# Kernel optimization log

Measured on AMD Instinct MI355X. Metric: run time of the kernel, lower is better.

The kernel has to match this reference:

```python
import jax, jax.numpy as jnp
import numpy as np

V, E = 4096, 8192
HV, HE, OUT = 256, 128, 256
EPS = 1e-6


def _one_hot_incidence(idx, n_rows, n_cols):
    # incidence matrix M[v, e] = 1 if idx[e] == v
    return jnp.zeros((n_rows, n_cols), jnp.float32).at[idx, jnp.arange(n_cols)].set(1.0)


def setup_inputs() -> dict:
    key = jax.random.key(0)
    ks = jax.random.split(key, 12)
    # edge endpoints: first V source indices cover every vertex -> positive degrees
    u_idx = jnp.concatenate([jnp.arange(V), jax.random.randint(ks[0], (E - V,), 0, V)])
    v_idx = jax.random.randint(ks[1], (E,), 0, V)
    vew1 = _one_hot_incidence(u_idx, V, E)
    vew2 = _one_hot_incidence(v_idx, V, E)
    hv_ftr = jax.random.normal(ks[2], (V, HV), jnp.float32)
    he_ftr = jax.random.normal(ks[3], (E, HE), jnp.float32)
    s = lambda d: 1.0 / np.sqrt(d)
    w_att = jax.random.normal(ks[4], (HV + HE + HV, 1), jnp.float32) * s(HV + HE + HV)
    b_att = jnp.zeros((1,), jnp.float32)
    w_gcn = jax.random.normal(ks[5], (HV, HV), jnp.float32) * s(HV)
    b_gcn = jnp.zeros((HV,), jnp.float32)
    w1 = jax.random.normal(ks[6], (2 * HV, HV), jnp.float32) * s(2 * HV)
    b1 = jnp.zeros((HV,), jnp.float32)
    w2 = jax.random.normal(ks[7], (HV, OUT), jnp.float32) * s(HV)
    b2 = jnp.zeros((OUT,), jnp.float32)
    return dict(hv_ftr=hv_ftr, he_ftr=he_ftr, vew1=vew1, vew2=vew2,
                w_att=w_att, b_att=b_att, w_gcn=w_gcn, b_gcn=b_gcn,
                w1=w1, b1=b1, w2=w2, b2=b2)


def reference(hv_ftr, he_ftr, vew1, vew2, w_att, b_att, w_gcn, b_gcn, w1, b1, w2, b2):
    vew_u = jnp.concatenate([vew1, vew2], axis=1)  # [V, 2E]
    vew_v = jnp.concatenate([vew2, vew1], axis=1)  # [V, 2E]
    hv_u = vew_u.T @ hv_ftr                         # [2E, HV] gather of source feats
    hv_v = vew_v.T @ hv_ftr                         # [2E, HV] gather of target feats
    he2 = jnp.concatenate([he_ftr, he_ftr], axis=0)  # [2E, HE]
    uev = jnp.concatenate([hv_u, he2, hv_v], axis=1)  # [2E, 2HV+HE]
    edge_w = jax.nn.sigmoid(uev @ w_att + b_att).reshape(-1)  # [2E]
    adj = vew_u @ (vew_v * edge_w[None, :]).T       # [V, V]
    # normalize_adj_rc: D_r^{-1/2} A D_c^{-1/2}
    d_r = jax.lax.rsqrt(jnp.maximum(adj.sum(axis=1), EPS))
    d_c = jax.lax.rsqrt(jnp.maximum(adj.sum(axis=0), EPS))
    adj_n = adj * d_r[:, None] * d_c[None, :]
    # GCN(hv_dim->hv_dim, tanh): propagate linear-transformed features
    hidden = jnp.tanh(adj_n @ (hv_ftr @ w_gcn + b_gcn))  # [V, HV]
    # MLP remap: [hv, hidden] -> hidden_dim HV -> OUT (dropout off at inference)
    h = jnp.concatenate([hv_ftr, hidden], axis=1)   # [V, 2HV]
    h = jax.nn.leaky_relu(h @ w1 + b1)
    return h @ w2 + b2                               # [V, OUT]
```

## Files before the change

kernel.cpp:

```cpp
#include <hip/hip_runtime.h>
#include <hip/hip_bf16.h>
#include <math.h>

#define V 4096
#define E 8192
#define HV 256
#define HE 128
#define OUT_DIM 256
#define EPS 1e-6f

typedef __attribute__((ext_vector_type(8))) short short8;
typedef __attribute__((ext_vector_type(4))) float f32x4;

__device__ __forceinline__ unsigned short f2bf(float f) {
    __hip_bfloat16 h = __float2bfloat16(f);
    return *(unsigned short*)&h;
}

__global__ __launch_bounds__(256) void zero_kernel(float4* __restrict__ p, int n4) {
    int i = blockIdx.x * blockDim.x + threadIdx.x;
    int stride = gridDim.x * blockDim.x;
    float4 z = {0.0f, 0.0f, 0.0f, 0.0f};
    for (; i < n4; i += stride) p[i] = z;
}

__global__ __launch_bounds__(256) void idx_kernel(const float4* __restrict__ m,
                                                  int* __restrict__ out) {
    const int EQ = E / 4;
    const size_t total = (size_t)V * EQ;
    for (size_t i = (size_t)blockIdx.x * blockDim.x + threadIdx.x; i < total;
         i += (size_t)gridDim.x * blockDim.x) {
        float4 x = m[i];
        if (x.x + x.y + x.z + x.w > 0.5f) {
            int v  = (int)(i / EQ);
            int c4 = (int)(i % EQ) * 4;
            if (x.x > 0.5f) out[c4 + 0] = v;
            if (x.y > 0.5f) out[c4 + 1] = v;
            if (x.z > 0.5f) out[c4 + 2] = v;
            if (x.w > 0.5f) out[c4 + 3] = v;
        }
    }
}

__global__ __launch_bounds__(256) void conv_kernel(const float4* __restrict__ src,
                                                   ushort4* __restrict__ dst, int n4) {
    int i = blockIdx.x * blockDim.x + threadIdx.x;
    int stride = gridDim.x * blockDim.x;
    for (; i < n4; i += stride) {
        float4 x = src[i];
        ushort4 o;
        o.x = f2bf(x.x); o.y = f2bf(x.y); o.z = f2bf(x.z); o.w = f2bf(x.w);
        dst[i] = o;
    }
}

__global__ __launch_bounds__(256) void convT_kernel(const float* __restrict__ src,
                                                    unsigned short* __restrict__ dst,
                                                    int K, int N) {
    int i = blockIdx.x * blockDim.x + threadIdx.x;
    if (i >= N * K) return;
    int n = i / K, k = i - n * K;
    dst[i] = f2bf(src[(size_t)k * N + n]);
}

__global__ __launch_bounds__(64) void proj_kernel(const float* __restrict__ hv,
                                                  const float* __restrict__ he,
                                                  const float* __restrict__ watt,
                                                  float* __restrict__ pu,
                                                  float* __restrict__ pv,
                                                  float* __restrict__ pe) {
    int r = blockIdx.x;
    int lane = threadIdx.x;
    if (r < V) {
        float4 x  = *(const float4*)(hv + (size_t)r * HV + lane * 4);
        float4 wu = *(const float4*)(watt + lane * 4);
        float4 wv = *(const float4*)(watt + HV + HE + lane * 4);
        float su = x.x * wu.x + x.y * wu.y + x.z * wu.z + x.w * wu.w;
        float sv = x.x * wv.x + x.y * wv.y + x.z * wv.z + x.w * wv.w;
        #pragma unroll
        for (int o = 32; o > 0; o >>= 1) {
            su += __shfl_down(su, o);
            sv += __shfl_down(sv, o);
        }
        if (lane == 0) { pu[r] = su; pv[r] = sv; }
    } else {
        int e = r - V;
        float2 x = *(const float2*)(he + (size_t)e * HE + lane * 2);
        float2 w = *(const float2*)(watt + HV + lane * 2);
        float s = x.x * w.x + x.y * w.y;
        #pragma unroll
        for (int o = 32; o > 0; o >>= 1) s += __shfl_down(s, o);
        if (lane == 0) pe[e] = s;
    }
}

__global__ __launch_bounds__(256) void edge_kernel(const int* __restrict__ iu,
                                                   const int* __restrict__ iv,
                                                   const float* __restrict__ pu,
                                                   const float* __restrict__ pv,
                                                   const float* __restrict__ pe,
                                                   const float* __restrict__ batt,
                                                   float* __restrict__ ew,
                                                   float* __restrict__ dr,
                                                   float* __restrict__ dc) {
    int e2 = blockIdx.x * blockDim.x + threadIdx.x;
    if (e2 >= 2 * E) return;
    int e  = (e2 < E) ? e2 : e2 - E;
    int uu = (e2 < E) ? iu[e] : iv[e];
    int vv = (e2 < E) ? iv[e] : iu[e];
    float x = pu[uu] + pe[e] + pv[vv] + batt[0];
    float w = 1.0f / (1.0f + expf(-x));
    ew[e2] = w;
    atomicAdd(dr + uu, w);
    atomicAdd(dc + vv, w);
}

template <int ACT, int OBF>
__global__ __launch_bounds__(256) void gemm_bf16(const unsigned short* __restrict__ A0,
                                                 const unsigned short* __restrict__ A1,
                                                 int KSEG, int NSEG,
                                                 const unsigned short* __restrict__ BT,
                                                 const float* __restrict__ bias,
                                                 void* __restrict__ Cout,
                                                 int M, int N) {
    __shared__ __align__(16) unsigned short As[64 * 40];
    __shared__ __align__(16) unsigned short Bs[64 * 40];
    const int tid  = threadIdx.x;
    const int lane = tid & 63;
    const int w    = tid >> 6;
    const int wm   = w >> 1, wn = w & 1;
    const int bm   = blockIdx.y * 64, bn = blockIdx.x * 64;
    const int Ktot = KSEG * NSEG;

    const int sr = tid >> 2;
    const int sc = (tid & 3) * 8;
    const int fr = lane & 15;
    const int kc = (lane >> 4) * 8;

    f32x4 acc[2][2] = {};

    for (int k0 = 0; k0 < Ktot; k0 += 32) {
        int seg = (k0 >= KSEG) ? 1 : 0;
        int kk  = k0 - seg * KSEG;
        const unsigned short* Asrc = seg ? A1 : A0;
        *(short8*)&As[sr * 40 + sc] = *(const short8*)&Asrc[(size_t)(bm + sr) * KSEG + kk + sc];
        *(short8*)&Bs[sr * 40 + sc] = *(const short8*)&BT[(size_t)(bn + sr) * Ktot + k0 + sc];
        __syncthreads();
        short8 bfr[2];
        bfr[0] = *(const short8*)&Bs[(wn * 32 + 0 * 16 + fr) * 40 + kc];
        bfr[1] = *(const short8*)&Bs[(wn * 32 + 1 * 16 + fr) * 40 + kc];
        #pragma unroll
        for (int ms = 0; ms < 2; ++ms) {
            short8 af = *(const short8*)&As[(wm * 32 + ms * 16 + fr) * 40 + kc];
            acc[ms][0] = __builtin_amdgcn_mfma_f32_16x16x32_bf16(af, bfr[0], acc[ms][0], 0, 0, 0);
            acc[ms][1] = __builtin_amdgcn_mfma_f32_16x16x32_bf16(af, bfr[1], acc[ms][1], 0, 0, 0);
        }
        __syncthreads();
    }

    #pragma unroll
    for (int ms = 0; ms < 2; ++ms) {
        #pragma unroll
        for (int ns = 0; ns < 2; ++ns) {
            int col = bn + wn * 32 + ns * 16 + fr;
            float bv = bias ? bias[col] : 0.0f;
            #pragma unroll
            for (int r = 0; r < 4; ++r) {
                int row = bm + wm * 32 + ms * 16 + ((lane >> 4) << 2) + r;
                float v = acc[ms][ns][r] + bv;
                if (ACT == 1) v = (v > 0.0f) ? v : 0.01f * v;
                if (OBF) ((unsigned short*)Cout)[(size_t)row * N + col] = f2bf(v);
                else     ((float*)Cout)[(size_t)row * N + col] = v;
            }
        }
    }
}

__global__ __launch_bounds__(64) void scatter_kernel(const int* __restrict__ iu,
                                                     const int* __restrict__ iv,
                                                     const float* __restrict__ ew,
                                                     const float* __restrict__ dc,
                                                     const float* __restrict__ X,
                                                     float* __restrict__ acc) {
    int e2 = blockIdx.x;
    int t  = threadIdx.x;
    int e  = (e2 < E) ? e2 : e2 - E;
    int uu = (e2 < E) ? iu[e] : iv[e];
    int vv = (e2 < E) ? iv[e] : iu[e];
    float coef = ew[e2] * rsqrtf(fmaxf(dc[vv], EPS));
    float4 x = *(const float4*)(X + (size_t)vv * HV + t * 4);
    float* dst = acc + (size_t)uu * HV + t * 4;
    atomicAdd(dst + 0, coef * x.x);
    atomicAdd(dst + 1, coef * x.y);
    atomicAdd(dst + 2, coef * x.z);
    atomicAdd(dst + 3, coef * x.w);
}

__global__ __launch_bounds__(256) void finish_kernel(const float* __restrict__ dr,
                                                     const float* __restrict__ acc,
                                                     unsigned short* __restrict__ hid16) {
    const size_t total = (size_t)V * HV;
    for (size_t idx = (size_t)blockIdx.x * blockDim.x + threadIdx.x; idx < total;
         idx += (size_t)gridDim.x * blockDim.x) {
        int row = (int)(idx >> 8);
        float s = rsqrtf(fmaxf(dr[row], EPS));
        hid16[idx] = f2bf(tanhf(s * acc[idx]));
    }
}

extern "C" void kernel_launch(void* const* d_in, const int* in_sizes, int n_in,
                              void* d_out, int out_size, void* d_ws, size_t ws_size,
                              hipStream_t stream) {
    const float* hv   = (const float*)d_in[0];
    const float* he   = (const float*)d_in[1];
    const float* vew1 = (const float*)d_in[2];
    const float* vew2 = (const float*)d_in[3];
    const float* watt = (const float*)d_in[4];
    const float* batt = (const float*)d_in[5];
    const float* wgcn = (const float*)d_in[6];
    const float* bgcn = (const float*)d_in[7];
    const float* w1   = (const float*)d_in[8];
    const float* b1   = (const float*)d_in[9];
    const float* w2   = (const float*)d_in[10];
    const float* b2   = (const float*)d_in[11];
    float* out = (float*)d_out;

    float* ws = (float*)d_ws;
    int*   iu  = (int*)ws;
    int*   iv  = (int*)(ws + E);
    float* pu  = ws + 2 * E;
    float* pv  = pu + V;
    float* pe  = pv + V;
    float* ew  = pe + E;
    float* dr  = ew + 2 * E;
    float* dc  = dr + V;
    float* acc = dc + V;
    float* X   = acc + (size_t)V * HV;
    unsigned short* hv16  = (unsigned short*)(X + (size_t)V * HV);
    unsigned short* hid16 = hv16 + (size_t)V * HV;
    unsigned short* t16   = hid16 + (size_t)V * HV;
    unsigned short* wgcnT = t16 + (size_t)V * HV;
    unsigned short* w1T   = wgcnT + HV * HV;
    unsigned short* w2T   = w1T + 2 * HV * HV;

    zero_kernel<<<1024, 256, 0, stream>>>((float4*)dr, (2 * V + V * HV) / 4);

    idx_kernel<<<2048, 256, 0, stream>>>((const float4*)vew1, iu);
    idx_kernel<<<2048, 256, 0, stream>>>((const float4*)vew2, iv);

    conv_kernel<<<512, 256, 0, stream>>>((const float4*)hv, (ushort4*)hv16, V * HV / 4);
    convT_kernel<<<(HV * HV + 255) / 256, 256, 0, stream>>>(wgcn, wgcnT, HV, HV);
    convT_kernel<<<(2 * HV * HV + 255) / 256, 256, 0, stream>>>(w1, w1T, 2 * HV, HV);
    convT_kernel<<<(HV * OUT_DIM + 255) / 256, 256, 0, stream>>>(w2, w2T, HV, OUT_DIM);

    proj_kernel<<<V + E, 64, 0, stream>>>(hv, he, watt, pu, pv, pe);
    edge_kernel<<<(2 * E + 255) / 256, 256, 0, stream>>>(iu, iv, pu, pv, pe, batt, ew, dr, dc);

    gemm_bf16<0, 0><<<dim3(HV / 64, V / 64), 256, 0, stream>>>(hv16, hv16, HV, 1, wgcnT, bgcn, X, V, HV);

    scatter_kernel<<<2 * E, 64, 0, stream>>>(iu, iv, ew, dc, X, acc);

    finish_kernel<<<1024, 256, 0, stream>>>(dr, acc, hid16);

    gemm_bf16<1, 1><<<dim3(HV / 64, V / 64), 256, 0, stream>>>(hv16, hid16, HV, 2, w1T, b1, t16, V, HV);

    gemm_bf16<0, 0><<<dim3(OUT_DIM / 64, V / 64), 256, 0, stream>>>(t16, t16, HV, 1, w2T, b2, out, V, OUT_DIM);
}
```

Measured before the change: 150.9 us.

## Fuse prologue kernels into one launch and convert fp32 to bf16 inside GEMM loads

Merges zeroing, incidence-index extraction, attention projections and the first GEMM into a single block-partitioned kernel, so they run concurrently and use fewer launches. The separate bf16 conversion and weight-transpose kernels are removed; the GEMMs now read fp32 operands directly and convert to bf16 while staging them into shared memory, transposing B during the LDS store. Intermediate activations stay fp32, which saves conversion passes but doubles the bytes each GEMM reads. The scalar transposed LDS stores may add bank conflicts.

```diff
diff --git a/kernel.cpp b/kernel.cpp
--- a/kernel.cpp
+++ b/kernel.cpp
@@ -9,6 +9,12 @@
 #define OUT_DIM 256
 #define EPS 1e-6f
 
+#define G_GEMM1 256
+#define G_PROJ  512
+#define G_ZERO  64
+#define G_IDX   8192
+#define G_TOTAL (G_GEMM1 + G_PROJ + G_ZERO + G_IDX)
+
 typedef __attribute__((ext_vector_type(8))) short short8;
 typedef __attribute__((ext_vector_type(4))) float f32x4;
 
@@ -17,80 +23,156 @@
     return *(unsigned short*)&h;
 }
 
-__global__ __launch_bounds__(256) void zero_kernel(float4* __restrict__ p, int n4) {
-    int i = blockIdx.x * blockDim.x + threadIdx.x;
-    int stride = gridDim.x * blockDim.x;
-    float4 z = {0.0f, 0.0f, 0.0f, 0.0f};
-    for (; i < n4; i += stride) p[i] = z;
-}
-
-__global__ __launch_bounds__(256) void idx_kernel(const float4* __restrict__ m,
-                                                  int* __restrict__ out) {
-    const int EQ = E / 4;
-    const size_t total = (size_t)V * EQ;
-    for (size_t i = (size_t)blockIdx.x * blockDim.x + threadIdx.x; i < total;
-         i += (size_t)gridDim.x * blockDim.x) {
-        float4 x = m[i];
-        if (x.x + x.y + x.z + x.w > 0.5f) {
-            int v  = (int)(i / EQ);
-            int c4 = (int)(i % EQ) * 4;
-            if (x.x > 0.5f) out[c4 + 0] = v;
-            if (x.y > 0.5f) out[c4 + 1] = v;
-            if (x.z > 0.5f) out[c4 + 2] = v;
-            if (x.w > 0.5f) out[c4 + 3] = v;
-        }
+__device__ __forceinline__ short8 cvt8(float4 a, float4 b) {
+    short8 r;
+    r[0] = f2bf(a.x); r[1] = f2bf(a.y); r[2] = f2bf(a.z); r[3] = f2bf(a.w);
+    r[4] = f2bf(b.x); r[5] = f2bf(b.y); r[6] = f2bf(b.z); r[7] = f2bf(b.w);
+    return r;
+}
+
+template <int ACT>
+__device__ __forceinline__ void gemm_body(const float* __restrict__ A0,
+                                          const float* __restrict__ A1,
+                                          int KSEG, int NSEG,
+                                          const float* __restrict__ B,
+                                          const float* __restrict__ bias,
+                                          float* __restrict__ Cout,
+                                          int N, int bm, int bn) {
+    __shared__ __align__(16) unsigned short As[64 * 40];
+    __shared__ __align__(16) unsigned short Bs[64 * 40];
+    const int tid  = threadIdx.x;
+    const int lane = tid & 63;
+    const int w    = tid >> 6;
+    const int wm   = w >> 1, wn = w & 1;
+    const int Ktot = KSEG * NSEG;
+
+    const int sr  = tid >> 2;
+    const int sc8 = (tid & 3) * 8;
+    const int kb  = tid & 31;
+    const int bc0 = (tid >> 5) * 8;
+    const int fr  = lane & 15;
+    const int kc  = (lane >> 4) * 8;
+
+    f32x4 acc[2][2] = {};
+
+    for (int k0 = 0; k0 < Ktot; k0 += 32) {
+        const float* Asrc = (k0 >= KSEG) ? A1 : A0;
+        int kk = (k0 >= KSEG) ? (k0 - KSEG) : k0;
+        const float* ap = &Asrc[(size_t)(bm + sr) * KSEG + kk + sc8];
+        float4 a0 = *(const float4*)ap;
+        float4 a1 = *(const float4*)(ap + 4);
+        const float* bp = &B[(size_t)(k0 + kb) * N + bn + bc0];
+        float4 b0 = *(const float4*)bp;
+        float4 b1 = *(const float4*)(bp + 4);
+        *(short8*)&As[sr * 40 + sc8] = cvt8(a0, a1);
+        unsigned short bw[8];
+        bw[0] = f2bf(b0.x); bw[1] = f2bf(b0.y); bw[2] = f2bf(b0.z); bw[3] = f2bf(b0.w);
+        bw[4] = f2bf(b1.x); bw[5] = f2bf(b1.y); bw[6] = f2bf(b1.z); bw[7] = f2bf(b1.w);
+        #pragma unroll
+        for (int j = 0; j < 8; ++j) Bs[(bc0 + j) * 40 + kb] = bw[j];
+        __syncthreads();
+
+        short8 bfr[2];
+        bfr[0] = *(const short8*)&Bs[(wn * 32 + 0 * 16 + fr) * 40 + kc];
+        bfr[1] = *(const short8*)&Bs[(wn * 32 + 1 * 16 + fr) * 40 + kc];
+        #pragma unroll
+        for (int ms = 0; ms < 2; ++ms) {
+            short8 af = *(const short8*)&As[(wm * 32 + ms * 16 + fr) * 40 + kc];
+            acc[ms][0] = __builtin_amdgcn_mfma_f32_16x16x32_bf16(af, bfr[0], acc[ms][0], 0, 0, 0);
+            acc[ms][1] = __builtin_amdgcn_mfma_f32_16x16x32_bf16(af, bfr[1], acc[ms][1], 0, 0, 0);
+        }
+        __syncthreads();
     }
-}
-
-__global__ __launch_bounds__(256) void conv_kernel(const float4* __restrict__ src,
-                                                   ushort4* __restrict__ dst, int n4) {
-    int i = blockIdx.x * blockDim.x + threadIdx.x;
-    int stride = gridDim.x * blockDim.x;
-    for (; i < n4; i += stride) {
-        float4 x = src[i];
-        ushort4 o;
-        o.x = f2bf(x.x); o.y = f2bf(x.y); o.z = f2bf(x.z); o.w = f2bf(x.w);
-        dst[i] = o;
+
+    #pragma unroll
+    for (int ms = 0; ms < 2; ++ms) {
+        #pragma unroll
+        for (int ns = 0; ns < 2; ++ns) {
+            int col = bn + wn * 32 + ns * 16 + fr;
+            float bv = bias ? bias[col] : 0.0f;
+            #pragma unroll
+            for (int r = 0; r < 4; ++r) {
+                int row = bm + wm * 32 + ms * 16 + ((lane >> 4) << 2) + r;
+                float v = acc[ms][ns][r] + bv;
+                if (ACT == 1) v = (v > 0.0f) ? v : 0.01f * v;
+                Cout[(size_t)row * N + col] = v;
+            }
+        }
     }
 }
 
-__global__ __launch_bounds__(256) void convT_kernel(const float* __restrict__ src,
-                                                    unsigned short* __restrict__ dst,
-                                                    int K, int N) {
-    int i = blockIdx.x * blockDim.x + threadIdx.x;
-    if (i >= N * K) return;
-    int n = i / K, k = i - n * K;
-    dst[i] = f2bf(src[(size_t)k * N + n]);
-}
-
-__global__ __launch_bounds__(64) void proj_kernel(const float* __restrict__ hv,
-                                                  const float* __restrict__ he,
-                                                  const float* __restrict__ watt,
-                                                  float* __restrict__ pu,
-                                                  float* __restrict__ pv,
-                                                  float* __restrict__ pe) {
-    int r = blockIdx.x;
-    int lane = threadIdx.x;
-    if (r < V) {
-        float4 x  = *(const float4*)(hv + (size_t)r * HV + lane * 4);
-        float4 wu = *(const float4*)(watt + lane * 4);
-        float4 wv = *(const float4*)(watt + HV + HE + lane * 4);
-        float su = x.x * wu.x + x.y * wu.y + x.z * wu.z + x.w * wu.w;
-        float sv = x.x * wv.x + x.y * wv.y + x.z * wv.z + x.w * wv.w;
-        #pragma unroll
-        for (int o = 32; o > 0; o >>= 1) {
-            su += __shfl_down(su, o);
-            sv += __shfl_down(sv, o);
-        }
-        if (lane == 0) { pu[r] = su; pv[r] = sv; }
+template <int ACT>
+__global__ __launch_bounds__(256) void gemm_kernel(const float* __restrict__ A0,
+                                                   const float* __restrict__ A1,
+                                                   int KSEG, int NSEG,
+                                                   const float* __restrict__ B,
+                                                   const float* __restrict__ bias,
+                                                   float* __restrict__ C, int N) {
+    gemm_body<ACT>(A0, A1, KSEG, NSEG, B, bias, C, N, blockIdx.y * 64, blockIdx.x * 64);
+}
+
+__global__ __launch_bounds__(256) void mega_kernel(
+    const float* __restrict__ hv, const float* __restrict__ he,
+    const float4* __restrict__ vew1, const float4* __restrict__ vew2,
+    const float* __restrict__ watt,
+    const float* __restrict__ wgcn, const float* __restrict__ bgcn,
+    int* __restrict__ iu, int* __restrict__ iv,
+    float* __restrict__ pu, float* __restrict__ pv, float* __restrict__ pe,
+    float4* __restrict__ zbase, int zn4,
+    float* __restrict__ X) {
+    const int b = blockIdx.x;
+    const int tid = threadIdx.x;
+
+    if (b < G_GEMM1) {
+        gemm_body<0>(hv, hv, HV, 1, wgcn, bgcn, X, HV, (b >> 2) * 64, (b & 3) * 64);
+    } else if (b < G_GEMM1 + G_PROJ) {
+        const int lane = tid & 63;
+        for (int r = (b - G_GEMM1) * 4 + (tid >> 6); r < V + E; r += G_PROJ * 4) {
+            if (r < V) {
+                float4 x  = *(const float4*)(hv + (size_t)r * HV + lane * 4);
+                float4 wu = *(const float4*)(watt + lane * 4);
+                float4 wv = *(const float4*)(watt + HV + HE + lane * 4);
+                float su = x.x * wu.x + x.y * wu.y + x.z * wu.z + x.w * wu.w;
+                float sv = x.x * wv.x + x.y * wv.y + x.z * wv.z + x.w * wv.w;
+                #pragma unroll
+                for (int o = 32; o > 0; o >>= 1) {
+                    su += __shfl_down(su, o);
+                    sv += __shfl_down(sv, o);
+                }
+                if (lane == 0) { pu[r] = su; pv[r] = sv; }
+            } else {
+                int e = r - V;
+                float2 x = *(const float2*)(he + (size_t)e * HE + lane * 2);
+                float2 w = *(const float2*)(watt + HV + lane * 2);
+                float s = x.x * w.x + x.y * w.y;
+                #pragma unroll
+                for (int o = 32; o > 0; o >>= 1) s += __shfl_down(s, o);
+                if (lane == 0) pe[e] = s;
+            }
+        }
+    } else if (b < G_GEMM1 + G_PROJ + G_ZERO) {
+        float4 z = {0.0f, 0.0f, 0.0f, 0.0f};
+        for (int i = (b - G_GEMM1 - G_PROJ) * 256 + tid; i < zn4; i += G_ZERO * 256)
+            zbase[i] = z;
     } else {
-        int e = r - V;
-        float2 x = *(const float2*)(he + (size_t)e * HE + lane * 2);
-        float2 w = *(const float2*)(watt + HV + lane * 2);
-        float s = x.x * w.x + x.y * w.y;
-        #pragma unroll
-        for (int o = 32; o > 0; o >>= 1) s += __shfl_down(s, o);
-        if (lane == 0) pe[e] = s;
+        int ib = b - (G_GEMM1 + G_PROJ + G_ZERO);
+        const float4* m = (ib < G_IDX / 2) ? vew1 : vew2;
+        int* o = (ib < G_IDX / 2) ? iu : iv;
+        ib &= (G_IDX / 2 - 1);
+        size_t base = (size_t)ib * 2048 + tid;
+        #pragma unroll
+        for (int it = 0; it < 8; ++it) {
+            size_t i = base + (size_t)it * 256;
+            float4 x = m[i];
+            if (x.x + x.y + x.z + x.w > 0.5f) {
+                int v  = (int)(i >> 11);
+                int c4 = ((int)i & 2047) << 2;
+                if (x.x > 0.5f) o[c4 + 0] = v;
+                if (x.y > 0.5f) o[c4 + 1] = v;
+                if (x.z > 0.5f) o[c4 + 2] = v;
+                if (x.w > 0.5f) o[c4 + 3] = v;
+            }
+        }
     }
 }
 
@@ -115,67 +197,6 @@
     atomicAdd(dc + vv, w);
 }
 
-template <int ACT, int OBF>
-__global__ __launch_bounds__(256) void gemm_bf16(const unsigned short* __restrict__ A0,
-                                                 const unsigned short* __restrict__ A1,
-                                                 int KSEG, int NSEG,
-                                                 const unsigned short* __restrict__ BT,
-                                                 const float* __restrict__ bias,
-                                                 void* __restrict__ Cout,
-                                                 int M, int N) {
-    __shared__ __align__(16) unsigned short As[64 * 40];
-    __shared__ __align__(16) unsigned short Bs[64 * 40];
-    const int tid  = threadIdx.x;
-    const int lane = tid & 63;
-    const int w    = tid >> 6;
-    const int wm   = w >> 1, wn = w & 1;
-    const int bm   = blockIdx.y * 64, bn = blockIdx.x * 64;
-    const int Ktot = KSEG * NSEG;
-
-    const int sr = tid >> 2;
-    const int sc = (tid & 3) * 8;
-    const int fr = lane & 15;
-    const int kc = (lane >> 4) * 8;
-
-    f32x4 acc[2][2] = {};
-
-    for (int k0 = 0; k0 < Ktot; k0 += 32) {
-        int seg = (k0 >= KSEG) ? 1 : 0;
-        int kk  = k0 - seg * KSEG;
-        const unsigned short* Asrc = seg ? A1 : A0;
-        *(short8*)&As[sr * 40 + sc] = *(const short8*)&Asrc[(size_t)(bm + sr) * KSEG + kk + sc];
-        *(short8*)&Bs[sr * 40 + sc] = *(const short8*)&BT[(size_t)(bn + sr) * Ktot + k0 + sc];
-        __syncthreads();
-        short8 bfr[2];
-        bfr[0] = *(const short8*)&Bs[(wn * 32 + 0 * 16 + fr) * 40 + kc];
-        bfr[1] = *(const short8*)&Bs[(wn * 32 + 1 * 16 + fr) * 40 + kc];
-        #pragma unroll
-        for (int ms = 0; ms < 2; ++ms) {
-            short8 af = *(const short8*)&As[(wm * 32 + ms * 16 + fr) * 40 + kc];
-            acc[ms][0] = __builtin_amdgcn_mfma_f32_16x16x32_bf16(af, bfr[0], acc[ms][0], 0, 0, 0);
-            acc[ms][1] = __builtin_amdgcn_mfma_f32_16x16x32_bf16(af, bfr[1], acc[ms][1], 0, 0, 0);
-        }
-        __syncthreads();
-    }
-
-    #pragma unroll
-    for (int ms = 0; ms < 2; ++ms) {
-        #pragma unroll
-        for (int ns = 0; ns < 2; ++ns) {
-            int col = bn + wn * 32 + ns * 16 + fr;
-            float bv = bias ? bias[col] : 0.0f;
-            #pragma unroll
-            for (int r = 0; r < 4; ++r) {
-                int row = bm + wm * 32 + ms * 16 + ((lane >> 4) << 2) + r;
-                float v = acc[ms][ns][r] + bv;
-                if (ACT == 1) v = (v > 0.0f) ? v : 0.01f * v;
-                if (OBF) ((unsigned short*)Cout)[(size_t)row * N + col] = f2bf(v);
-                else     ((float*)Cout)[(size_t)row * N + col] = v;
-            }
-        }
-    }
-}
-
 __global__ __launch_bounds__(64) void scatter_kernel(const int* __restrict__ iu,
                                                      const int* __restrict__ iv,
                                                      const float* __restrict__ ew,
@@ -197,15 +218,14 @@
 }
 
 __global__ __launch_bounds__(256) void finish_kernel(const float* __restrict__ dr,
-                                                     const float* __restrict__ acc,
-                                                     unsigned short* __restrict__ hid16) {
-    const size_t total = (size_t)V * HV;
-    for (size_t idx = (size_t)blockIdx.x * blockDim.x + threadIdx.x; idx < total;
-         idx += (size_t)gridDim.x * blockDim.x) {
-        int row = (int)(idx >> 8);
-        float s = rsqrtf(fmaxf(dr[row], EPS));
-        hid16[idx] = f2bf(tanhf(s * acc[idx]));
-    }
+                                                     float4* __restrict__ acc) {
+    int i = blockIdx.x * 256 + threadIdx.x;
+    int row = i >> 6;
+    float s = rsqrtf(fmaxf(dr[row], EPS));
+    float4 x = acc[i];
+    x.x = tanhf(s * x.x); x.y = tanhf(s * x.y);
+    x.z = tanhf(s * x.z); x.w = tanhf(s * x.w);
+    acc[i] = x;
 }
 
 extern "C" void kernel_launch(void* const* d_in, const int* in_sizes, int n_in,
@@ -236,33 +256,20 @@
     float* dc  = dr + V;
     float* acc = dc + V;
     float* X   = acc + (size_t)V * HV;
-    unsigned short* hv16  = (unsigned short*)(X + (size_t)V * HV);
-    unsigned short* hid16 = hv16 + (size_t)V * HV;
-    unsigned short* t16   = hid16 + (size_t)V * HV;
-    unsigned short* wgcnT = t16 + (size_t)V * HV;
-    unsigned short* w1T   = wgcnT + HV * HV;
-    unsigned short* w2T   = w1T + 2 * HV * HV;
-
-    zero_kernel<<<1024, 256, 0, stream>>>((float4*)dr, (2 * V + V * HV) / 4);
-
-    idx_kernel<<<2048, 256, 0, stream>>>((const float4*)vew1, iu);
-    idx_kernel<<<2048, 256, 0, stream>>>((const float4*)vew2, iv);
-
-    conv_kernel<<<512, 256, 0, stream>>>((const float4*)hv, (ushort4*)hv16, V * HV / 4);
-    convT_kernel<<<(HV * HV + 255) / 256, 256, 0, stream>>>(wgcn, wgcnT, HV, HV);
-    convT_kernel<<<(2 * HV * HV + 255) / 256, 256, 0, stream>>>(w1, w1T, 2 * HV, HV);
-    convT_kernel<<<(HV * OUT_DIM + 255) / 256, 256, 0, stream>>>(w2, w2T, HV, OUT_DIM);
-
-    proj_kernel<<<V + E, 64, 0, stream>>>(hv, he, watt, pu, pv, pe);
+
+    const int zn4 = (2 * V + V * HV) / 4;
+
+    mega_kernel<<<G_TOTAL, 256, 0, stream>>>(hv, he, (const float4*)vew1,
+        (const float4*)vew2, watt, wgcn, bgcn, iu, iv, pu, pv, pe,
+        (float4*)dr, zn4, X);
+
     edge_kernel<<<(2 * E + 255) / 256, 256, 0, stream>>>(iu, iv, pu, pv, pe, batt, ew, dr, dc);
 
-    gemm_bf16<0, 0><<<dim3(HV / 64, V / 64), 256, 0, stream>>>(hv16, hv16, HV, 1, wgcnT, bgcn, X, V, HV);
-
     scatter_kernel<<<2 * E, 64, 0, stream>>>(iu, iv, ew, dc, X, acc);
 
-    finish_kernel<<<1024, 256, 0, stream>>>(dr, acc, hid16);
-
-    gemm_bf16<1, 1><<<dim3(HV / 64, V / 64), 256, 0, stream>>>(hv16, hid16, HV, 2, w1T, b1, t16, V, HV);
-
-    gemm_bf16<0, 0><<<dim3(OUT_DIM / 64, V / 64), 256, 0, stream>>>(t16, t16, HV, 1, w2T, b2, out, V, OUT_DIM);
-}
+    finish_kernel<<<V * HV / 4 / 256, 256, 0, stream>>>(dr, (float4*)acc);
+
+    gemm_kernel<1><<<dim3(HV / 64, V / 64), 256, 0, stream>>>(hv, acc, HV, 2, w1, b1, X, HV);
+
+    gemm_kernel<0><<<dim3(OUT_DIM / 64, V / 64), 256, 0, stream>>>(X, X, HV, 1, w2, b2, out, OUT_DIM);
+}
```

Measured after the change: 135.6 us (median of 2 runs). -10.1%, faster.
